# Kernel tuning notes

Hardware: AMD Instinct MI355X
Metric: run time of the kernel (lower is better)

## Reference

```python
import jax, jax.numpy as jnp
import numpy as np

N, D, NBINS, NUM_IDS = 8192, 256, 64, 512
MAX_DIST = 2.0  # initial +/- histogram range from __init__ (max_dist default)
EPS_DIST = 1e-12
EPS_HIST = 1e-6


def setup_inputs() -> dict:
    key = jax.random.key(0)
    kx, kt = jax.random.split(key)
    x = jax.random.normal(kx, (N, D), dtype=jnp.float32)
    targets = jax.random.randint(kt, (N,), 0, NUM_IDS, dtype=jnp.int64)
    histogram = jnp.ones((NBINS,), dtype=jnp.float32)  # buffer initial state
    return {"x": x, "targets": targets, "histogram": histogram}


def reference(x, targets, histogram):
    n = x.shape[0]
    nbins = histogram.shape[0]
    # pairwise euclidean distances: [n, n]
    sq = jnp.sum(x * x, axis=1)
    dist = jnp.sqrt(jnp.clip(sq[:, None] + sq[None, :] - 2.0 * (x @ x.T), EPS_DIST, None))
    mask = targets[:, None] == targets[None, :]
    neg_inf = jnp.array(-jnp.inf, dtype=dist.dtype)
    pos_inf = jnp.array(jnp.inf, dtype=dist.dtype)
    pos_dist = jnp.max(jnp.where(mask, dist, neg_inf), axis=1)  # hardest positive per row
    neg_dist = jnp.min(jnp.where(mask, pos_inf, dist), axis=1)  # hardest negative per row
    hist_val = pos_dist - neg_dist
    # _compute_histogram: widen range by batch extremes (torch uses .item() on detached values)
    hv = jax.lax.stop_gradient(hist_val)
    max_val = jnp.maximum(jnp.max(hv), MAX_DIST)
    min_val = jnp.minimum(jnp.min(hv), -MAX_DIST)
    bin_width = (max_val - min_val) / (nbins - 1)
    lo = jnp.floor((hv - min_val) / bin_width).astype(jnp.int32)
    hi = jnp.clip(lo + 1, 0, nbins - 1)
    alpha = 1.0 - (hv - min_val - lo.astype(hv.dtype) * bin_width) / bin_width
    hist = jnp.zeros((nbins,), dtype=hv.dtype).at[lo].add(alpha).at[hi].add(1.0 - alpha)
    hist = hist / (jnp.sum(hist) + EPS_HIST)
    # first call: _stats_initialized is False -> momentum = 1.0, new buffer = hist
    new_histogram = hist
    pdf = new_histogram / jnp.sum(new_histogram)
    cdf = jnp.cumsum(pdf)
    bin_idx = jnp.floor((hv - min_val) / bin_width).astype(jnp.int32)
    weight = cdf[bin_idx]  # detached weighting (built entirely from stop_gradient values)
    loss = -jnp.mean(neg_dist * weight) + jnp.mean(pos_dist * weight)
    return loss
```

## Files before the change

### kernel.cpp

```cpp
#include <hip/hip_runtime.h>
#include <math.h>

#define Nn 8192
#define Dd 256
#define NBINS 64
#define NSPLIT 8

typedef __attribute__((ext_vector_type(8))) short short8;
typedef __attribute__((ext_vector_type(4))) float f32x4;

#define GLOAD16(g, l)                                                        \
  __builtin_amdgcn_global_load_lds(                                          \
      (const __attribute__((address_space(1))) void*)(g),                    \
      (__attribute__((address_space(3))) void*)(l), 16, 0, 0)

static __device__ __forceinline__ unsigned short f2bf(float f) {
  unsigned int u = __float_as_uint(f);
  u = (u + 0x7fffu + ((u >> 16) & 1u)) >> 16;
  return (unsigned short)u;
}
static __device__ __forceinline__ unsigned int enc_ord(float f) {
  unsigned int u = __float_as_uint(f);
  return (u & 0x80000000u) ? ~u : (u | 0x80000000u);
}
static __device__ __forceinline__ float dec_ord(unsigned int u) {
  unsigned int b2 = (u & 0x80000000u) ? (u ^ 0x80000000u) : ~u;
  return __uint_as_float(b2);
}

__global__ __launch_bounds__(256) void prep_kernel(const float* __restrict__ x,
                                                   const int* __restrict__ lab,
                                                   unsigned short* __restrict__ xb,
                                                   float2* __restrict__ sqlab,
                                                   unsigned int* __restrict__ pos2,
                                                   unsigned int* __restrict__ neg2,
                                                   unsigned int* __restrict__ gmm,
                                                   float* __restrict__ ghist,
                                                   float* __restrict__ ghsum,
                                                   unsigned int* __restrict__ cnt) {
  const int w = threadIdx.x >> 6;
  const int lane = threadIdx.x & 63;
  const int row = blockIdx.x * 4 + w;
  const float4 v = *(const float4*)(x + (size_t)row * Dd + lane * 4);
  ushort4 b;
  b.x = f2bf(v.x); b.y = f2bf(v.y); b.z = f2bf(v.z); b.w = f2bf(v.w);
  *(ushort4*)(xb + (size_t)row * Dd + lane * 4) = b;
  float s = v.x * v.x + v.y * v.y + v.z * v.z + v.w * v.w;
#pragma unroll
  for (int off = 32; off >= 1; off >>= 1) s += __shfl_xor(s, off);
  if (lane == 0) {
    sqlab[row] = make_float2(s, __int_as_float(lab[row]));
    pos2[row] = 0x007fffffu;
    neg2[row] = 0xff800000u;
  }
  if (blockIdx.x == 0 && threadIdx.x < NBINS) {
    ghist[threadIdx.x] = 0.0f;
    ghsum[threadIdx.x] = 0.0f;
    if (threadIdx.x == 0) { gmm[0] = 0x007fffffu; gmm[1] = 0xff800000u; cnt[0] = 0u; }
  }
}

static __device__ __forceinline__ void stage_a(const unsigned short* __restrict__ xb,
                                               int r0, int hh, unsigned short* buf, int t) {
#pragma unroll
  for (int i = 0; i < 8; ++i) {
    const int c = i * 256 + t;
    const int col = c >> 4;
    const int kq = (c & 15) ^ (col & 15);
    GLOAD16(xb + (size_t)(r0 + col) * Dd + hh * 128 + kq * 8, buf + (size_t)c * 8);
  }
}
static __device__ __forceinline__ void stage_b(const unsigned short* __restrict__ xb,
                                               int c0, int hh, unsigned short* buf, int t) {
#pragma unroll
  for (int i = 0; i < 4; ++i) {
    const int c = i * 256 + t;
    const int col = c >> 4;
    const int kq = (c & 15) ^ (col & 15);
    GLOAD16(xb + (size_t)(c0 + col) * Dd + hh * 128 + kq * 8, buf + (size_t)c * 8);
  }
}

__global__ __launch_bounds__(256, 2) void pairwise_kernel(const unsigned short* __restrict__ xb,
                                                          const float2* __restrict__ sqlab,
                                                          unsigned int* __restrict__ pos2,
                                                          unsigned int* __restrict__ neg2) {
  __shared__ __align__(16) unsigned short Us[4096 * 8];
  __shared__ __align__(16) float2 sl_s[1024];
  __shared__ int lab_s[128];

  const int t = threadIdx.x;
  const int lane = t & 63;
  const int w = t >> 6;
  const int wr = w >> 1;
  const int wc = w & 1;
  const int c_l = lane & 15;
  const int kq_l = lane >> 4;
  const int rows0 = blockIdx.x * 128;
  const int cbase = blockIdx.y * (Nn / NSPLIT);

  stage_a(xb, rows0, 0, Us, t);
  stage_a(xb, rows0, 1, Us + 2048 * 8, t);
#pragma unroll
  for (int i = 0; i < 4; ++i) sl_s[i * 256 + t] = sqlab[cbase + i * 256 + t];
  if (t < 128) lab_s[t] = __float_as_int(sqlab[rows0 + t].y);
  __syncthreads();

  const short8* Uv = (const short8*)Us;
  short8 af[32];
#pragma unroll
  for (int k2 = 0; k2 < 8; ++k2)
#pragma unroll
    for (int m = 0; m < 4; ++m) {
      const int kqf = k2 * 4 + kq_l;
      const int rl = wr * 64 + m * 16 + c_l;
      af[k2 * 4 + m] = Uv[(kqf >> 4) * 2048 + rl * 16 + ((kqf & 15) ^ (rl & 15))];
    }
  int labp[8];
#pragma unroll
  for (int m = 0; m < 4; ++m)
#pragma unroll
    for (int pp = 0; pp < 2; ++pp) {
      const int r0 = wr * 64 + m * 16 + kq_l * 4 + 2 * pp;
      labp[m * 2 + pp] = (lab_s[r0] & 0xffff) | (lab_s[r0 + 1] << 16);
    }
  __syncthreads();

  unsigned short* const Bs0 = Us;
  unsigned short* const Bs1 = Us + 2048 * 8;

  stage_b(xb, cbase, 0, Bs0, t);
  stage_b(xb, cbase, 1, Bs0 + 1024 * 8, t);

  const int cc0 = wc * 32 + c_l;
  const int cc1 = wc * 32 + 16 + c_l;
  const int x0 = cc0 & 15, x1 = cc1 & 15;
  float pmax[16], nmin[16];
#pragma unroll
  for (int i = 0; i < 16; ++i) { pmax[i] = -INFINITY; nmin[i] = INFINITY; }

#pragma unroll 1
  for (int ct2 = 0; ct2 < 8; ++ct2) {
#pragma unroll
    for (int half = 0; half < 2; ++half) {
      const int ct = 2 * ct2 + half;
      const unsigned short* const bufR = half ? Bs1 : Bs0;
      unsigned short* const bufW = half ? Bs0 : Bs1;

      __syncthreads();
      if (ct < 15) {
        stage_b(xb, cbase + (ct + 1) * 64, 0, bufW, t);
        stage_b(xb, cbase + (ct + 1) * 64, 1, bufW + 1024 * 8, t);
      }

      f32x4 acc[4][2];
#pragma unroll
      for (int m = 0; m < 4; ++m)
#pragma unroll
        for (int n = 0; n < 2; ++n) acc[m][n] = (f32x4){0.f, 0.f, 0.f, 0.f};

      const short8* const Bv0 = (const short8*)bufR;
      const short8* const Bv1 = (const short8*)(bufR + 1024 * 8);

#pragma unroll
      for (int ks = 0; ks < 8; ++ks) {
        const short8* const B = (ks < 4) ? Bv0 : Bv1;
        const int o = (ks & 3) * 4 + kq_l;
        const short8 bf0 = B[cc0 * 16 + (o ^ x0)];
#pragma unroll
        for (int m = 0; m < 4; ++m)
          acc[m][0] = __builtin_amdgcn_mfma_f32_16x16x32_bf16(af[ks * 4 + m], bf0, acc[m][0], 0, 0, 0);
      }
#pragma unroll
      for (int ks = 0; ks < 8; ++ks) {
        const short8* const B = (ks < 4) ? Bv0 : Bv1;
        const int o = (ks & 3) * 4 + kq_l;
        const short8 bf1 = B[cc1 * 16 + (o ^ x1)];
#pragma unroll
        for (int m = 0; m < 4; ++m)
          acc[m][1] = __builtin_amdgcn_mfma_f32_16x16x32_bf16(af[ks * 4 + m], bf1, acc[m][1], 0, 0, 0);
      }

      const float2 sl0 = sl_s[ct * 64 + cc0];
      const int lc0 = __float_as_int(sl0.y);
#pragma unroll
      for (int idx = 0; idx < 16; ++idx) {
        const int m = idx >> 2, q = idx & 3;
        const int lr = (labp[idx >> 1] >> ((idx & 1) * 16)) & 0xffff;
        const float g0 = fmaf(-2.0f, acc[m][0][q], sl0.x);
        const bool s0 = (lr == lc0);
        pmax[idx] = fmaxf(pmax[idx], s0 ? g0 : -INFINITY);
        nmin[idx] = fminf(nmin[idx], s0 ? INFINITY : g0);
      }
      const float2 sl1 = sl_s[ct * 64 + cc1];
      const int lc1 = __float_as_int(sl1.y);
#pragma unroll
      for (int idx = 0; idx < 16; ++idx) {
        const int m = idx >> 2, q = idx & 3;
        const int lr = (labp[idx >> 1] >> ((idx & 1) * 16)) & 0xffff;
        const float g1 = fmaf(-2.0f, acc[m][1][q], sl1.x);
        const bool s1 = (lr == lc1);
        pmax[idx] = fmaxf(pmax[idx], s1 ? g1 : -INFINITY);
        nmin[idx] = fminf(nmin[idx], s1 ? INFINITY : g1);
      }
    }
  }

#pragma unroll
  for (int i = 0; i < 16; ++i) {
    float p = pmax[i], nn2 = nmin[i];
#pragma unroll
    for (int off = 1; off < 16; off <<= 1) {
      p = fmaxf(p, __shfl_xor(p, off));
      nn2 = fminf(nn2, __shfl_xor(nn2, off));
    }
    if (c_l == 0) {
      const int rowg = rows0 + wr * 64 + (i >> 2) * 16 + kq_l * 4 + (i & 3);
      atomicMax(&pos2[rowg], enc_ord(p));
      atomicMin(&neg2[rowg], enc_ord(nn2));
    }
  }
}

__global__ __launch_bounds__(512) void finalize_a_kernel(const float2* __restrict__ sqlab,
                                                         const unsigned int* __restrict__ pos2,
                                                         const unsigned int* __restrict__ neg2,
                                                         float* __restrict__ hv_g,
                                                         unsigned int* __restrict__ gmm) {
  const int i = blockIdx.x * 512 + threadIdx.x;
  const int lane = threadIdx.x & 63;
  const float s = sqlab[i].x;
  const float p2 = fmaxf(s + dec_ord(pos2[i]), 1e-12f);
  const float n2 = fmaxf(s + dec_ord(neg2[i]), 1e-12f);
  const float hv = sqrtf(p2) - sqrtf(n2);
  hv_g[i] = hv;
  float lmax = hv, lmin = hv;
#pragma unroll
  for (int off = 32; off >= 1; off >>= 1) {
    lmax = fmaxf(lmax, __shfl_xor(lmax, off));
    lmin = fminf(lmin, __shfl_xor(lmin, off));
  }
  if (lane == 0) {
    atomicMax(&gmm[0], enc_ord(lmax));
    atomicMin(&gmm[1], enc_ord(lmin));
  }
}

__global__ __launch_bounds__(512) void finalize_b_kernel(const float* __restrict__ hv_g,
                                                         const unsigned int* __restrict__ gmm,
                                                         float* __restrict__ ghist,
                                                         float* __restrict__ ghsum,
                                                         unsigned int* __restrict__ cnt,
                                                         float* __restrict__ out) {
  __shared__ float hist_s[NBINS];
  __shared__ float hsum_s[NBINS];
  __shared__ unsigned int s_last;
  const int t = threadIdx.x;
  if (t < NBINS) { hist_s[t] = 0.0f; hsum_s[t] = 0.0f; }
  const float maxv = fmaxf(dec_ord(gmm[0]), 2.0f);
  const float minv = fminf(dec_ord(gmm[1]), -2.0f);
  const float bw = (maxv - minv) / (float)(NBINS - 1);
  __syncthreads();

  const int i = blockIdx.x * 512 + t;
  const float hv = hv_g[i];
  int lo = (int)floorf((hv - minv) / bw);
  lo = min(max(lo, 0), NBINS - 1);
  const int hi = min(lo + 1, NBINS - 1);
  const float alpha = 1.0f - (hv - minv - (float)lo * bw) / bw;
  atomicAdd(&hist_s[lo], alpha);
  atomicAdd(&hist_s[hi], 1.0f - alpha);
  atomicAdd(&hsum_s[lo], hv);
  __syncthreads();

  if (t < NBINS) {
    atomicAdd(&ghist[t], hist_s[t]);
    atomicAdd(&ghsum[t], hsum_s[t]);
  }
  __threadfence();
  if (t == 0) s_last = atomicAdd(cnt, 1u);
  __syncthreads();
  if (s_last != (unsigned int)(gridDim.x - 1)) return;

  if (t < NBINS) {
    const float h = __hip_atomic_load(&ghist[t], __ATOMIC_RELAXED, __HIP_MEMORY_SCOPE_AGENT);
    const float hs = __hip_atomic_load(&ghsum[t], __ATOMIC_RELAXED, __HIP_MEMORY_SCOPE_AGENT);
    float total = h;
#pragma unroll
    for (int off = 32; off >= 1; off >>= 1) total += __shfl_xor(total, off);
    const float hn = h / (total + 1e-6f);
    float s2 = hn;
#pragma unroll
    for (int off = 32; off >= 1; off >>= 1) s2 += __shfl_xor(s2, off);
    const float pdf = hn / s2;
    float c = pdf;
#pragma unroll
    for (int off = 1; off < 64; off <<= 1) {
      const float u = __shfl_up(c, off);
      if (t >= off) c += u;
    }
    float acc = c * hs;
#pragma unroll
    for (int off = 32; off >= 1; off >>= 1) acc += __shfl_xor(acc, off);
    if (t == 0) out[0] = acc / (float)Nn;
  }
}

extern "C" void kernel_launch(void* const* d_in, const int* in_sizes, int n_in,
                              void* d_out, int out_size, void* d_ws, size_t ws_size,
                              hipStream_t stream) {
  const float* x = (const float*)d_in[0];
  const int* targets = (const int*)d_in[1];
  float* out = (float*)d_out;

  char* p = (char*)d_ws;
  unsigned short* xb = (unsigned short*)p;  p += (size_t)Nn * Dd * 2;
  float2* sqlab = (float2*)p;               p += (size_t)Nn * 8;
  unsigned int* pos2 = (unsigned int*)p;    p += (size_t)Nn * 4;
  unsigned int* neg2 = (unsigned int*)p;    p += (size_t)Nn * 4;
  float* hv_g = (float*)p;                  p += (size_t)Nn * 4;
  unsigned int* gmm = (unsigned int*)p;     p += 64;
  float* ghist = (float*)p;                 p += NBINS * 4;
  float* ghsum = (float*)p;                 p += NBINS * 4;
  unsigned int* cnt = (unsigned int*)p;

  prep_kernel<<<Nn / 4, 256, 0, stream>>>(x, targets, xb, sqlab, pos2, neg2, gmm, ghist, ghsum, cnt);
  pairwise_kernel<<<dim3(Nn / 128, NSPLIT), 256, 0, stream>>>(xb, sqlab, pos2, neg2);
  finalize_a_kernel<<<Nn / 512, 512, 0, stream>>>(sqlab, pos2, neg2, hv_g, gmm);
  finalize_b_kernel<<<Nn / 512, 512, 0, stream>>>(hv_g, gmm, ghist, ghsum, cnt, out);
}
```

Measured before the change: 62.34 us.

## Fuse finalize kernels with last-block histogram and raise MFMA wave priority

Merges the two finalize kernels into one. Each block computes its hv values and global min/max, then the last block to finish (tracked by an atomic counter) builds the whole histogram from hv_g using per-wave shared-memory bins and computes the loss. This removes one kernel launch and the global histogram atomics, at the cost of a serial 8192-element histogram pass in a single block. It also raises wave priority with s_setprio around the MFMA loops in the pairwise kernel.

New measurement: 100.2 us. 60.7% more time.

```diff
diff --git a/kernel.cpp b/kernel.cpp
--- a/kernel.cpp
+++ b/kernel.cpp
@@ -35,8 +35,6 @@
                                                    unsigned int* __restrict__ pos2,
                                                    unsigned int* __restrict__ neg2,
                                                    unsigned int* __restrict__ gmm,
-                                                   float* __restrict__ ghist,
-                                                   float* __restrict__ ghsum,
                                                    unsigned int* __restrict__ cnt) {
   const int w = threadIdx.x >> 6;
   const int lane = threadIdx.x & 63;
@@ -53,10 +51,8 @@
     pos2[row] = 0x007fffffu;
     neg2[row] = 0xff800000u;
   }
-  if (blockIdx.x == 0 && threadIdx.x < NBINS) {
-    ghist[threadIdx.x] = 0.0f;
-    ghsum[threadIdx.x] = 0.0f;
-    if (threadIdx.x == 0) { gmm[0] = 0x007fffffu; gmm[1] = 0xff800000u; cnt[0] = 0u; }
+  if (blockIdx.x == 0 && threadIdx.x == 0) {
+    gmm[0] = 0x007fffffu; gmm[1] = 0xff800000u; cnt[0] = 0u;
   }
 }
 
@@ -162,6 +158,7 @@
       const short8* const Bv0 = (const short8*)bufR;
       const short8* const Bv1 = (const short8*)(bufR + 1024 * 8);
 
+      __builtin_amdgcn_s_setprio(1);
 #pragma unroll
       for (int ks = 0; ks < 8; ++ks) {
         const short8* const B = (ks < 4) ? Bv0 : Bv1;
@@ -180,6 +177,7 @@
         for (int m = 0; m < 4; ++m)
           acc[m][1] = __builtin_amdgcn_mfma_f32_16x16x32_bf16(af[ks * 4 + m], bf1, acc[m][1], 0, 0, 0);
       }
+      __builtin_amdgcn_s_setprio(0);
 
       const float2 sl0 = sl_s[ct * 64 + cc0];
       const int lc0 = __float_as_int(sl0.y);
@@ -222,13 +220,21 @@
   }
 }
 
-__global__ __launch_bounds__(512) void finalize_a_kernel(const float2* __restrict__ sqlab,
-                                                         const unsigned int* __restrict__ pos2,
-                                                         const unsigned int* __restrict__ neg2,
-                                                         float* __restrict__ hv_g,
-                                                         unsigned int* __restrict__ gmm) {
-  const int i = blockIdx.x * 512 + threadIdx.x;
-  const int lane = threadIdx.x & 63;
+__global__ __launch_bounds__(512) void finalize_kernel(const float2* __restrict__ sqlab,
+                                                       const unsigned int* __restrict__ pos2,
+                                                       const unsigned int* __restrict__ neg2,
+                                                       float* __restrict__ hv_g,
+                                                       unsigned int* __restrict__ gmm,
+                                                       unsigned int* __restrict__ cnt,
+                                                       float* __restrict__ out) {
+  __shared__ float hist_w[8][NBINS];
+  __shared__ float hsum_w[8][NBINS];
+  __shared__ float cdf_s[NBINS];
+  __shared__ unsigned int s_last;
+  const int t = threadIdx.x;
+  const int lane = t & 63, wv = t >> 6;
+
+  const int i = blockIdx.x * 512 + t;
   const float s = sqlab[i].x;
   const float p2 = fmaxf(s + dec_ord(pos2[i]), 1e-12f);
   const float n2 = fmaxf(s + dec_ord(neg2[i]), 1e-12f);
@@ -244,47 +250,38 @@
     atomicMax(&gmm[0], enc_ord(lmax));
     atomicMin(&gmm[1], enc_ord(lmin));
   }
-}
-
-__global__ __launch_bounds__(512) void finalize_b_kernel(const float* __restrict__ hv_g,
-                                                         const unsigned int* __restrict__ gmm,
-                                                         float* __restrict__ ghist,
-                                                         float* __restrict__ ghsum,
-                                                         unsigned int* __restrict__ cnt,
-                                                         float* __restrict__ out) {
-  __shared__ float hist_s[NBINS];
-  __shared__ float hsum_s[NBINS];
-  __shared__ unsigned int s_last;
-  const int t = threadIdx.x;
-  if (t < NBINS) { hist_s[t] = 0.0f; hsum_s[t] = 0.0f; }
-  const float maxv = fmaxf(dec_ord(gmm[0]), 2.0f);
-  const float minv = fminf(dec_ord(gmm[1]), -2.0f);
+  __threadfence();
+  __syncthreads();
+  if (t == 0) s_last = atomicAdd(cnt, 1u);
+  __syncthreads();
+  if (s_last != (unsigned int)(gridDim.x - 1)) return;
+
+  const unsigned int gmx = __hip_atomic_load(&gmm[0], __ATOMIC_RELAXED, __HIP_MEMORY_SCOPE_AGENT);
+  const unsigned int gmn = __hip_atomic_load(&gmm[1], __ATOMIC_RELAXED, __HIP_MEMORY_SCOPE_AGENT);
+  const float maxv = fmaxf(dec_ord(gmx), 2.0f);
+  const float minv = fminf(dec_ord(gmn), -2.0f);
   const float bw = (maxv - minv) / (float)(NBINS - 1);
-  __syncthreads();
-
-  const int i = blockIdx.x * 512 + t;
-  const float hv = hv_g[i];
-  int lo = (int)floorf((hv - minv) / bw);
-  lo = min(max(lo, 0), NBINS - 1);
-  const int hi = min(lo + 1, NBINS - 1);
-  const float alpha = 1.0f - (hv - minv - (float)lo * bw) / bw;
-  atomicAdd(&hist_s[lo], alpha);
-  atomicAdd(&hist_s[hi], 1.0f - alpha);
-  atomicAdd(&hsum_s[lo], hv);
+  hist_w[wv][lane] = 0.0f;
+  hsum_w[wv][lane] = 0.0f;
+  __syncthreads();
+
+  for (int j = t; j < Nn; j += 512) {
+    const float h = __uint_as_float(
+        __hip_atomic_load((const unsigned int*)&hv_g[j], __ATOMIC_RELAXED, __HIP_MEMORY_SCOPE_AGENT));
+    int lo = (int)floorf((h - minv) / bw);
+    lo = min(max(lo, 0), NBINS - 1);
+    const int hi = min(lo + 1, NBINS - 1);
+    const float alpha = 1.0f - (h - minv - (float)lo * bw) / bw;
+    atomicAdd(&hist_w[wv][lo], alpha);
+    atomicAdd(&hist_w[wv][hi], 1.0f - alpha);
+    atomicAdd(&hsum_w[wv][lo], h);
+  }
   __syncthreads();
 
   if (t < NBINS) {
-    atomicAdd(&ghist[t], hist_s[t]);
-    atomicAdd(&ghsum[t], hsum_s[t]);
-  }
-  __threadfence();
-  if (t == 0) s_last = atomicAdd(cnt, 1u);
-  __syncthreads();
-  if (s_last != (unsigned int)(gridDim.x - 1)) return;
-
-  if (t < NBINS) {
-    const float h = __hip_atomic_load(&ghist[t], __ATOMIC_RELAXED, __HIP_MEMORY_SCOPE_AGENT);
-    const float hs = __hip_atomic_load(&ghsum[t], __ATOMIC_RELAXED, __HIP_MEMORY_SCOPE_AGENT);
+    float h = 0.0f, hs = 0.0f;
+#pragma unroll
+    for (int w2 = 0; w2 < 8; ++w2) { h += hist_w[w2][t]; hs += hsum_w[w2][t]; }
     float total = h;
 #pragma unroll
     for (int off = 32; off >= 1; off >>= 1) total += __shfl_xor(total, off);
@@ -320,12 +317,9 @@
   unsigned int* neg2 = (unsigned int*)p;    p += (size_t)Nn * 4;
   float* hv_g = (float*)p;                  p += (size_t)Nn * 4;
   unsigned int* gmm = (unsigned int*)p;     p += 64;
-  float* ghist = (float*)p;                 p += NBINS * 4;
-  float* ghsum = (float*)p;                 p += NBINS * 4;
   unsigned int* cnt = (unsigned int*)p;
 
-  prep_kernel<<<Nn / 4, 256, 0, stream>>>(x, targets, xb, sqlab, pos2, neg2, gmm, ghist, ghsum, cnt);
+  prep_kernel<<<Nn / 4, 256, 0, stream>>>(x, targets, xb, sqlab, pos2, neg2, gmm, cnt);
   pairwise_kernel<<<dim3(Nn / 128, NSPLIT), 256, 0, stream>>>(xb, sqlab, pos2, neg2);
-  finalize_a_kernel<<<Nn / 512, 512, 0, stream>>>(sqlab, pos2, neg2, hv_g, gmm);
-  finalize_b_kernel<<<Nn / 512, 512, 0, stream>>>(hv_g, gmm, ghist, ghsum, cnt, out);
-}
+  finalize_kernel<<<Nn / 512, 512, 0, stream>>>(sqlab, pos2, neg2, hv_g, gmm, cnt, out);
+}
```
